# Kernel optimization log

Measured on AMD Instinct MI355X. Metric: run time of the kernel, lower is better.

The kernel has to match this reference:

```python
import jax, jax.numpy as jnp
import numpy as np

N_NODES = 50000
N_EDGES = 640000
F_IN = 16
F_OUT = 16
FCH = 16


def setup_inputs() -> dict:
    key = jax.random.key(0)
    ks = jax.random.split(key, 8)
    x = jax.random.normal(ks[0], (N_NODES, F_IN), dtype=jnp.float32)
    edge_index = jax.random.randint(ks[1], (2, N_EDGES), 0, N_NODES, dtype=jnp.int64)
    edge_vec = jax.random.normal(ks[2], (N_EDGES, 3), dtype=jnp.float32)
    norm = jax.random.uniform(ks[3], (N_EDGES,), dtype=jnp.float32)
    # hypernetwork MLP params: Linear(3, fch) -> ReLU -> Linear(fch, 2*Fin*Fout)
    W1 = jax.random.normal(ks[4], (3, FCH), dtype=jnp.float32) / np.sqrt(3.0)
    b1 = jnp.zeros((FCH,), dtype=jnp.float32)
    W2 = jax.random.normal(ks[5], (FCH, 2 * F_IN * F_OUT), dtype=jnp.float32) / np.sqrt(FCH)
    b2 = jnp.zeros((2 * F_IN * F_OUT,), dtype=jnp.float32)
    return {"x": x, "edge_index": edge_index, "edge_vec": edge_vec, "norm": norm,
            "W1": W1, "b1": b1, "W2": W2, "b2": b2}


def reference(x, edge_index, edge_vec, norm, W1, b1, W2, b2):
    edge_src = edge_index[0]
    edge_dst = edge_index[1]
    # per-edge generated weight matrices: [E, F_OUT, 2*F_IN]
    h = jax.nn.relu(edge_vec @ W1 + b1)
    weights = (h @ W2 + b2).reshape(-1, F_OUT, 2 * F_IN)
    # gather endpoint features and concat: [E, 2*F_IN]
    xe = jnp.concatenate([x[edge_src], x[edge_dst]], axis=1)
    # batched small matmul, tanh activation, norm scaling: [E, F_OUT]
    edge_ftr = jnp.tanh(jnp.einsum('eoi,ei->eo', weights, xe)) * norm[:, None]
    # scatter-add into destination nodes
    return jax.ops.segment_sum(edge_ftr, edge_dst, num_segments=N_NODES)
```

## Files before the change

### kernel.cpp

```cpp
#include <hip/hip_runtime.h>
#include <hip/hip_bf16.h>

#define N_NODES 50000
#define N_EDGES 640000

typedef __attribute__((ext_vector_type(8))) short bf16x8;
typedef __attribute__((ext_vector_type(4))) float f32x4;

static __device__ __forceinline__ short f2bf(float f) {
    __hip_bfloat16 h = __float2bfloat16(f);
    return *reinterpret_cast<const short*>(&h);
}

static __device__ __forceinline__ float sgpr_f(const float* p) {
    return __uint_as_float(__builtin_amdgcn_readfirstlane(__float_as_uint(*p)));
}

__global__ __launch_bounds__(256)
void edge_hyper_kernel(const float* __restrict__ x,
                       const int* __restrict__ ei,
                       const float* __restrict__ ev,
                       const float* __restrict__ nrm,
                       const float* __restrict__ W1,
                       const float* __restrict__ b1,
                       const float* __restrict__ W2,
                       const float* __restrict__ b2,
                       float* __restrict__ out,
                       int ngroups)
{
    __shared__ short w2s[17 * 16 * 34];

    const int tid  = threadIdx.x;
    const int l    = tid & 63;
    const int r    = l & 15;
    const int half = l >> 4;

    for (int idx = tid; idx < 17 * 512; idx += 256) {
        const int c   = idx >> 9;
        const int rem = idx & 511;
        const int o   = rem >> 5;
        const int k   = rem & 31;
        const float v = (c < 16) ? W2[c * 512 + o * 32 + k] : b2[o * 32 + k];
        w2s[(c * 16 + o) * 34 + k] = f2bf(v);
    }

    float w1c0[16], w1c1[16], w1c2[16], b1s[16];
    #pragma unroll
    for (int c = 0; c < 16; ++c) {
        w1c0[c] = sgpr_f(W1 + c);
        w1c1[c] = sgpr_f(W1 + 16 + c);
        w1c2[c] = sgpr_f(W1 + 32 + c);
        b1s[c]  = sgpr_f(b1 + c);
    }

    __syncthreads();

    const short* wbase = &w2s[r * 34 + half * 8];

    const int wv = tid >> 6;
    int g = blockIdx.x * 4 + wv;
    const int nw = gridDim.x * 4;
    if (g >= ngroups) return;

    int    idx_c;
    float4 xa_c, xb_c, nr_c;
    int4   dst_c;
    {
        const int e0 = g * 16;
        idx_c = ei[(half >= 2 ? N_EDGES : 0) + e0 + r];
        nr_c  = *reinterpret_cast<const float4*>(nrm + e0 + half * 4);
        dst_c = *reinterpret_cast<const int4*>(ei + N_EDGES + e0 + half * 4);
        const float4* xr = reinterpret_cast<const float4*>(
            x + (size_t)idx_c * 16 + (half & 1) * 8);
        xa_c = xr[0];
        xb_c = xr[1];
    }

    while (g < ngroups) {
        const int gn   = g + nw;
        const bool hasn = gn < ngroups;
        const int e0   = g * 16;

        const float4* evp = reinterpret_cast<const float4*>(
            ev + (size_t)e0 * 3 + half * 12);
        const float4 ea = evp[0];
        const float4 eb = evp[1];
        const float4 ec = evp[2];

        int    idx_n = 0;
        float4 nr_n = {0.f, 0.f, 0.f, 0.f};
        int4   dst_n = {0, 0, 0, 0};
        if (hasn) {
            const int e0n = gn * 16;
            idx_n = ei[(half >= 2 ? N_EDGES : 0) + e0n + r];
            nr_n  = *reinterpret_cast<const float4*>(nrm + e0n + half * 4);
            dst_n = *reinterpret_cast<const int4*>(ei + N_EDGES + e0n + half * 4);
        }

        bf16x8 afrag;
        afrag[0] = f2bf(xa_c.x); afrag[1] = f2bf(xa_c.y);
        afrag[2] = f2bf(xa_c.z); afrag[3] = f2bf(xa_c.w);
        afrag[4] = f2bf(xb_c.x); afrag[5] = f2bf(xb_c.y);
        afrag[6] = f2bf(xb_c.z); afrag[7] = f2bf(xb_c.w);

        float4 xa_n = {0.f,0.f,0.f,0.f}, xb_n = {0.f,0.f,0.f,0.f};
        if (hasn) {
            const float4* xr = reinterpret_cast<const float4*>(
                x + (size_t)idx_n * 16 + (half & 1) * 8);
            xa_n = xr[0];
            xb_n = xr[1];
        }

        f32x4 s;
        {
            const bf16x8 bfr = *reinterpret_cast<const bf16x8*>(wbase + 16 * 544);
            s = __builtin_amdgcn_mfma_f32_16x16x32_bf16(
                afrag, bfr, (f32x4){0.f, 0.f, 0.f, 0.f}, 0, 0, 0);
        }

        const float ev0[4] = {ea.x, ea.w, eb.z, ec.y};
        const float ev1[4] = {ea.y, eb.x, eb.w, ec.z};
        const float ev2[4] = {ea.z, eb.y, ec.x, ec.w};

        #pragma unroll
        for (int c = 0; c < 16; ++c) {
            const bf16x8 bfr = *reinterpret_cast<const bf16x8*>(wbase + c * 544);
            f32x4 t = __builtin_amdgcn_mfma_f32_16x16x32_bf16(
                afrag, bfr, (f32x4){0.f, 0.f, 0.f, 0.f}, 0, 0, 0);
            #pragma unroll
            for (int q = 0; q < 4; ++q) {
                float hv = fmaf(ev2[q], w1c2[c],
                           fmaf(ev1[q], w1c1[c],
                           fmaf(ev0[q], w1c0[c], b1s[c])));
                hv = fmaxf(hv, 0.0f);
                s[q] = fmaf(hv, t[q], s[q]);
            }
        }

        const float nrv[4] = {nr_c.x, nr_c.y, nr_c.z, nr_c.w};
        const int   dsv[4] = {dst_c.x, dst_c.y, dst_c.z, dst_c.w};
        #pragma unroll
        for (int q = 0; q < 4; ++q) {
            const float sv = s[q];
            const float t  = __expf(-2.0f * fabsf(sv));
            const float th = copysignf((1.0f - t) * __builtin_amdgcn_rcpf(1.0f + t), sv);
            atomicAdd(out + (size_t)dsv[q] * 16 + r, th * nrv[q]);
        }

        idx_c = idx_n;
        nr_c  = nr_n;
        dst_c = dst_n;
        xa_c  = xa_n;
        xb_c  = xb_n;
        g = gn;
    }
}

extern "C" void kernel_launch(void* const* d_in, const int* in_sizes, int n_in,
                              void* d_out, int out_size, void* d_ws, size_t ws_size,
                              hipStream_t stream) {
    const float* x   = (const float*)d_in[0];
    const int*   ei  = (const int*)d_in[1];
    const float* ev  = (const float*)d_in[2];
    const float* nrm = (const float*)d_in[3];
    const float* W1  = (const float*)d_in[4];
    const float* b1  = (const float*)d_in[5];
    const float* W2  = (const float*)d_in[6];
    const float* b2  = (const float*)d_in[7];
    float* out = (float*)d_out;

    hipMemsetAsync(out, 0, (size_t)out_size * sizeof(float), stream);

    const int ngroups = N_EDGES / 16;
    dim3 grid(2048), block(256);
    hipLaunchKernelGGL(edge_hyper_kernel, grid, block, 0, stream,
                       x, ei, ev, nrm, W1, b1, W2, b2, out, ngroups);
}
```

Baseline: 60.30 us.

## Fold hidden activations into MFMA A-operand and accumulate in-chain

Moves the per-edge hidden activation h[c] from a post-MFMA scalar scaling step into the A fragment, so each lane scales its gathered x features by h[c] before the bf16 conversion and the MFMA accumulates directly. Two accumulators alternate to break the MFMA dependency chain. Edge vectors are now loaded per row and prefetched one iteration ahead, and the prefetch is made unconditional by clamping the next index. This removes the per-chunk 4x FMA combine but adds 8 multiplies and bf16 conversions per chunk, and rounds h*x to bf16, which changes precision.

```diff
diff --git a/kernel.cpp b/kernel.cpp
--- a/kernel.cpp
+++ b/kernel.cpp
@@ -63,11 +63,14 @@
     if (g >= ngroups) return;
 
     int    idx_c;
+    float  e0_c, e1_c, e2_c;
     float4 xa_c, xb_c, nr_c;
     int4   dst_c;
     {
         const int e0 = g * 16;
         idx_c = ei[(half >= 2 ? N_EDGES : 0) + e0 + r];
+        const float* evp = ev + (size_t)(e0 + r) * 3;
+        e0_c = evp[0]; e1_c = evp[1]; e2_c = evp[2];
         nr_c  = *reinterpret_cast<const float4*>(nrm + e0 + half * 4);
         dst_c = *reinterpret_cast<const int4*>(ei + N_EDGES + e0 + half * 4);
         const float4* xr = reinterpret_cast<const float4*>(
@@ -77,24 +80,23 @@
     }
 
     while (g < ngroups) {
-        const int gn   = g + nw;
-        const bool hasn = gn < ngroups;
-        const int e0   = g * 16;
+        const int gn    = g + nw;
+        const int gsafe = (gn < ngroups) ? gn : g;
 
-        const float4* evp = reinterpret_cast<const float4*>(
-            ev + (size_t)e0 * 3 + half * 12);
-        const float4 ea = evp[0];
-        const float4 eb = evp[1];
-        const float4 ec = evp[2];
+        const int e0n = gsafe * 16;
+        const int   idx_n = ei[(half >= 2 ? N_EDGES : 0) + e0n + r];
+        const float* evpn = ev + (size_t)(e0n + r) * 3;
+        const float e0_n = evpn[0], e1_n = evpn[1], e2_n = evpn[2];
+        const float4 nr_n = *reinterpret_cast<const float4*>(nrm + e0n + half * 4);
+        const int4   dst_n = *reinterpret_cast<const int4*>(ei + N_EDGES + e0n + half * 4);
 
-        int    idx_n = 0;
-        float4 nr_n = {0.f, 0.f, 0.f, 0.f};
-        int4   dst_n = {0, 0, 0, 0};
-        if (hasn) {
-            const int e0n = gn * 16;
-            idx_n = ei[(half >= 2 ? N_EDGES : 0) + e0n + r];
-            nr_n  = *reinterpret_cast<const float4*>(nrm + e0n + half * 4);
-            dst_n = *reinterpret_cast<const int4*>(ei + N_EDGES + e0n + half * 4);
+        float h[16];
+        #pragma unroll
+        for (int c = 0; c < 16; ++c) {
+            const float hv = fmaf(e2_c, w1c2[c],
+                             fmaf(e1_c, w1c1[c],
+                             fmaf(e0_c, w1c0[c], b1s[c])));
+            h[c] = fmaxf(hv, 0.0f);
         }
 
         bf16x8 afrag;
@@ -103,51 +105,50 @@
         afrag[4] = f2bf(xb_c.x); afrag[5] = f2bf(xb_c.y);
         afrag[6] = f2bf(xb_c.z); afrag[7] = f2bf(xb_c.w);
 
-        float4 xa_n = {0.f,0.f,0.f,0.f}, xb_n = {0.f,0.f,0.f,0.f};
-        if (hasn) {
-            const float4* xr = reinterpret_cast<const float4*>(
-                x + (size_t)idx_n * 16 + (half & 1) * 8);
-            xa_n = xr[0];
-            xb_n = xr[1];
-        }
+        const float4* xrn = reinterpret_cast<const float4*>(
+            x + (size_t)idx_n * 16 + (half & 1) * 8);
+        const float4 xa_n = xrn[0];
+        const float4 xb_n = xrn[1];
 
-        f32x4 s;
+        f32x4 accA, accB;
         {
             const bf16x8 bfr = *reinterpret_cast<const bf16x8*>(wbase + 16 * 544);
-            s = __builtin_amdgcn_mfma_f32_16x16x32_bf16(
+            accA = __builtin_amdgcn_mfma_f32_16x16x32_bf16(
                 afrag, bfr, (f32x4){0.f, 0.f, 0.f, 0.f}, 0, 0, 0);
         }
-
-        const float ev0[4] = {ea.x, ea.w, eb.z, ec.y};
-        const float ev1[4] = {ea.y, eb.x, eb.w, ec.z};
-        const float ev2[4] = {ea.z, eb.y, ec.x, ec.w};
+        accB = (f32x4){0.f, 0.f, 0.f, 0.f};
 
         #pragma unroll
         for (int c = 0; c < 16; ++c) {
             const bf16x8 bfr = *reinterpret_cast<const bf16x8*>(wbase + c * 544);
-            f32x4 t = __builtin_amdgcn_mfma_f32_16x16x32_bf16(
-                afrag, bfr, (f32x4){0.f, 0.f, 0.f, 0.f}, 0, 0, 0);
-            #pragma unroll
-            for (int q = 0; q < 4; ++q) {
-                float hv = fmaf(ev2[q], w1c2[c],
-                           fmaf(ev1[q], w1c1[c],
-                           fmaf(ev0[q], w1c0[c], b1s[c])));
-                hv = fmaxf(hv, 0.0f);
-                s[q] = fmaf(hv, t[q], s[q]);
-            }
+            const float hc = h[c];
+            const float4 y0 = make_float4(hc * xa_c.x, hc * xa_c.y,
+                                          hc * xa_c.z, hc * xa_c.w);
+            const float4 y1 = make_float4(hc * xb_c.x, hc * xb_c.y,
+                                          hc * xb_c.z, hc * xb_c.w);
+            bf16x8 yf;
+            yf[0] = f2bf(y0.x); yf[1] = f2bf(y0.y);
+            yf[2] = f2bf(y0.z); yf[3] = f2bf(y0.w);
+            yf[4] = f2bf(y1.x); yf[5] = f2bf(y1.y);
+            yf[6] = f2bf(y1.z); yf[7] = f2bf(y1.w);
+            if (c & 1)
+                accB = __builtin_amdgcn_mfma_f32_16x16x32_bf16(yf, bfr, accB, 0, 0, 0);
+            else
+                accA = __builtin_amdgcn_mfma_f32_16x16x32_bf16(yf, bfr, accA, 0, 0, 0);
         }
 
         const float nrv[4] = {nr_c.x, nr_c.y, nr_c.z, nr_c.w};
         const int   dsv[4] = {dst_c.x, dst_c.y, dst_c.z, dst_c.w};
         #pragma unroll
         for (int q = 0; q < 4; ++q) {
-            const float sv = s[q];
+            const float sv = accA[q] + accB[q];
             const float t  = __expf(-2.0f * fabsf(sv));
             const float th = copysignf((1.0f - t) * __builtin_amdgcn_rcpf(1.0f + t), sv);
             atomicAdd(out + (size_t)dsv[q] * 16 + r, th * nrv[q]);
         }
 
         idx_c = idx_n;
+        e0_c = e0_n; e1_c = e1_n; e2_c = e2_n;
         nr_c  = nr_n;
         dst_c = dst_n;
         xa_c  = xa_n;
```

Result: faster. 58.49 us (-3.0%).

## Process two edge groups per iteration with deeper index and feature prefetch

Applied to the files above, without the earlier changes.

Each wave now handles two 16-edge groups per loop iteration and interleaves their MFMA chains. Edge indices are prefetched two iterations ahead and gathered node features one iteration ahead. The goal is more memory-level parallelism and independent MFMA work to hide gather latency. The cost is higher register pressure, and out-of-range groups are clamped to valid ones and masked, which adds redundant loads at the tail.

```diff
diff --git a/kernel.cpp b/kernel.cpp
--- a/kernel.cpp
+++ b/kernel.cpp
@@ -58,102 +58,133 @@
     const short* wbase = &w2s[r * 34 + half * 8];
 
     const int wv = tid >> 6;
-    int g = blockIdx.x * 4 + wv;
     const int nw = gridDim.x * 4;
-    if (g >= ngroups) return;
-
-    int    idx_c;
-    float4 xa_c, xb_c, nr_c;
-    int4   dst_c;
+    const int gw = blockIdx.x * 4 + wv;
+    if (gw >= ngroups) return;
+    const int eisel = (half >= 2 ? N_EDGES : 0);
+
+    int gA = gw;
+    int gB = gw + nw;
+
+    #define CLAMPG(G) ((G) < ngroups ? (G) : gw)
+
+    int idxA = ei[eisel + gA * 16 + r];
+    int idxB = ei[eisel + CLAMPG(gB) * 16 + r];
+    float4 xaA, xbA, xaB, xbB;
     {
-        const int e0 = g * 16;
-        idx_c = ei[(half >= 2 ? N_EDGES : 0) + e0 + r];
-        nr_c  = *reinterpret_cast<const float4*>(nrm + e0 + half * 4);
-        dst_c = *reinterpret_cast<const int4*>(ei + N_EDGES + e0 + half * 4);
-        const float4* xr = reinterpret_cast<const float4*>(
-            x + (size_t)idx_c * 16 + (half & 1) * 8);
-        xa_c = xr[0];
-        xb_c = xr[1];
-    }
-
-    while (g < ngroups) {
-        const int gn   = g + nw;
-        const bool hasn = gn < ngroups;
-        const int e0   = g * 16;
-
-        const float4* evp = reinterpret_cast<const float4*>(
-            ev + (size_t)e0 * 3 + half * 12);
-        const float4 ea = evp[0];
-        const float4 eb = evp[1];
-        const float4 ec = evp[2];
-
-        int    idx_n = 0;
-        float4 nr_n = {0.f, 0.f, 0.f, 0.f};
-        int4   dst_n = {0, 0, 0, 0};
-        if (hasn) {
-            const int e0n = gn * 16;
-            idx_n = ei[(half >= 2 ? N_EDGES : 0) + e0n + r];
-            nr_n  = *reinterpret_cast<const float4*>(nrm + e0n + half * 4);
-            dst_n = *reinterpret_cast<const int4*>(ei + N_EDGES + e0n + half * 4);
-        }
-
-        bf16x8 afrag;
-        afrag[0] = f2bf(xa_c.x); afrag[1] = f2bf(xa_c.y);
-        afrag[2] = f2bf(xa_c.z); afrag[3] = f2bf(xa_c.w);
-        afrag[4] = f2bf(xb_c.x); afrag[5] = f2bf(xb_c.y);
-        afrag[6] = f2bf(xb_c.z); afrag[7] = f2bf(xb_c.w);
-
-        float4 xa_n = {0.f,0.f,0.f,0.f}, xb_n = {0.f,0.f,0.f,0.f};
-        if (hasn) {
-            const float4* xr = reinterpret_cast<const float4*>(
-                x + (size_t)idx_n * 16 + (half & 1) * 8);
-            xa_n = xr[0];
-            xb_n = xr[1];
-        }
-
-        f32x4 s;
+        const float4* p = reinterpret_cast<const float4*>(
+            x + (size_t)idxA * 16 + (half & 1) * 8);
+        xaA = p[0]; xbA = p[1];
+        const float4* q = reinterpret_cast<const float4*>(
+            x + (size_t)idxB * 16 + (half & 1) * 8);
+        xaB = q[0]; xbB = q[1];
+    }
+    int idxA1 = ei[eisel + CLAMPG(gA + 2 * nw) * 16 + r];
+    int idxB1 = ei[eisel + CLAMPG(gB + 2 * nw) * 16 + r];
+
+    while (gA < ngroups) {
+        const bool vB = (gB < ngroups);
+        const int gAs = gA;
+        const int gBs = CLAMPG(gB);
+
+        const int idxA2 = ei[eisel + CLAMPG(gA + 4 * nw) * 16 + r];
+        const int idxB2 = ei[eisel + CLAMPG(gB + 4 * nw) * 16 + r];
+
+        const float4* xp1 = reinterpret_cast<const float4*>(
+            x + (size_t)idxA1 * 16 + (half & 1) * 8);
+        const float4 xaA1 = xp1[0];
+        const float4 xbA1 = xp1[1];
+        const float4* xq1 = reinterpret_cast<const float4*>(
+            x + (size_t)idxB1 * 16 + (half & 1) * 8);
+        const float4 xaB1 = xq1[0];
+        const float4 xbB1 = xq1[1];
+
+        const float4* evpA = reinterpret_cast<const float4*>(
+            ev + (size_t)gAs * 48 + half * 12);
+        const float4 eaA = evpA[0], ebA = evpA[1], ecA = evpA[2];
+        const float4* evpB = reinterpret_cast<const float4*>(
+            ev + (size_t)gBs * 48 + half * 12);
+        const float4 eaB = evpB[0], ebB = evpB[1], ecB = evpB[2];
+        const float4 nrA = *reinterpret_cast<const float4*>(nrm + gAs * 16 + half * 4);
+        const float4 nrB = *reinterpret_cast<const float4*>(nrm + gBs * 16 + half * 4);
+        const int4  dstA = *reinterpret_cast<const int4*>(ei + N_EDGES + gAs * 16 + half * 4);
+        const int4  dstB = *reinterpret_cast<const int4*>(ei + N_EDGES + gBs * 16 + half * 4);
+
+        bf16x8 afA, afB;
+        afA[0] = f2bf(xaA.x); afA[1] = f2bf(xaA.y);
+        afA[2] = f2bf(xaA.z); afA[3] = f2bf(xaA.w);
+        afA[4] = f2bf(xbA.x); afA[5] = f2bf(xbA.y);
+        afA[6] = f2bf(xbA.z); afA[7] = f2bf(xbA.w);
+        afB[0] = f2bf(xaB.x); afB[1] = f2bf(xaB.y);
+        afB[2] = f2bf(xaB.z); afB[3] = f2bf(xaB.w);
+        afB[4] = f2bf(xbB.x); afB[5] = f2bf(xbB.y);
+        afB[6] = f2bf(xbB.z); afB[7] = f2bf(xbB.w);
+
+        f32x4 accA, accB;
         {
             const bf16x8 bfr = *reinterpret_cast<const bf16x8*>(wbase + 16 * 544);
-            s = __builtin_amdgcn_mfma_f32_16x16x32_bf16(
-                afrag, bfr, (f32x4){0.f, 0.f, 0.f, 0.f}, 0, 0, 0);
-        }
-
-        const float ev0[4] = {ea.x, ea.w, eb.z, ec.y};
-        const float ev1[4] = {ea.y, eb.x, eb.w, ec.z};
-        const float ev2[4] = {ea.z, eb.y, ec.x, ec.w};
+            accA = __builtin_amdgcn_mfma_f32_16x16x32_bf16(
+                afA, bfr, (f32x4){0.f, 0.f, 0.f, 0.f}, 0, 0, 0);
+            accB = __builtin_amdgcn_mfma_f32_16x16x32_bf16(
+                afB, bfr, (f32x4){0.f, 0.f, 0.f, 0.f}, 0, 0, 0);
+        }
+
+        const float evA0[4] = {eaA.x, eaA.w, ebA.z, ecA.y};
+        const float evA1[4] = {eaA.y, ebA.x, ebA.w, ecA.z};
+        const float evA2[4] = {eaA.z, ebA.y, ecA.x, ecA.w};
+        const float evB0[4] = {eaB.x, eaB.w, ebB.z, ecB.y};
+        const float evB1[4] = {eaB.y, ebB.x, ebB.w, ecB.z};
+        const float evB2[4] = {eaB.z, ebB.y, ecB.x, ecB.w};
 
         #pragma unroll
         for (int c = 0; c < 16; ++c) {
             const bf16x8 bfr = *reinterpret_cast<const bf16x8*>(wbase + c * 544);
-            f32x4 t = __builtin_amdgcn_mfma_f32_16x16x32_bf16(
-                afrag, bfr, (f32x4){0.f, 0.f, 0.f, 0.f}, 0, 0, 0);
+            const f32x4 tA = __builtin_amdgcn_mfma_f32_16x16x32_bf16(
+                afA, bfr, (f32x4){0.f, 0.f, 0.f, 0.f}, 0, 0, 0);
+            const f32x4 tB = __builtin_amdgcn_mfma_f32_16x16x32_bf16(
+                afB, bfr, (f32x4){0.f, 0.f, 0.f, 0.f}, 0, 0, 0);
             #pragma unroll
             for (int q = 0; q < 4; ++q) {
-                float hv = fmaf(ev2[q], w1c2[c],
-                           fmaf(ev1[q], w1c1[c],
-                           fmaf(ev0[q], w1c0[c], b1s[c])));
-                hv = fmaxf(hv, 0.0f);
-                s[q] = fmaf(hv, t[q], s[q]);
+                float hA = fmaf(evA2[q], w1c2[c],
+                           fmaf(evA1[q], w1c1[c],
+                           fmaf(evA0[q], w1c0[c], b1s[c])));
+                hA = fmaxf(hA, 0.0f);
+                accA[q] = fmaf(hA, tA[q], accA[q]);
+                float hB = fmaf(evB2[q], w1c2[c],
+                           fmaf(evB1[q], w1c1[c],
+                           fmaf(evB0[q], w1c0[c], b1s[c])));
+                hB = fmaxf(hB, 0.0f);
+                accB[q] = fmaf(hB, tB[q], accB[q]);
             }
         }
 
-        const float nrv[4] = {nr_c.x, nr_c.y, nr_c.z, nr_c.w};
-        const int   dsv[4] = {dst_c.x, dst_c.y, dst_c.z, dst_c.w};
         #pragma unroll
         for (int q = 0; q < 4; ++q) {
-            const float sv = s[q];
+            const float sv = accA[q];
             const float t  = __expf(-2.0f * fabsf(sv));
             const float th = copysignf((1.0f - t) * __builtin_amdgcn_rcpf(1.0f + t), sv);
-            atomicAdd(out + (size_t)dsv[q] * 16 + r, th * nrv[q]);
-        }
-
-        idx_c = idx_n;
-        nr_c  = nr_n;
-        dst_c = dst_n;
-        xa_c  = xa_n;
-        xb_c  = xb_n;
-        g = gn;
-    }
+            const float* nr4 = reinterpret_cast<const float*>(&nrA);
+            const int*   ds4 = reinterpret_cast<const int*>(&dstA);
+            atomicAdd(out + (size_t)ds4[q] * 16 + r, th * nr4[q]);
+        }
+        if (vB) {
+            #pragma unroll
+            for (int q = 0; q < 4; ++q) {
+                const float sv = accB[q];
+                const float t  = __expf(-2.0f * fabsf(sv));
+                const float th = copysignf((1.0f - t) * __builtin_amdgcn_rcpf(1.0f + t), sv);
+                const float* nr4 = reinterpret_cast<const float*>(&nrB);
+                const int*   ds4 = reinterpret_cast<const int*>(&dstB);
+                atomicAdd(out + (size_t)ds4[q] * 16 + r, th * nr4[q]);
+            }
+        }
+
+        xaA = xaA1; xbA = xbA1; xaB = xaB1; xbB = xbB1;
+        idxA1 = idxA2; idxB1 = idxB2;
+        gA += 2 * nw;
+        gB += 2 * nw;
+    }
+    #undef CLAMPG
 }
 
 extern "C" void kernel_launch(void* const* d_in, const int* in_sizes, int n_in,
```

New measurement: 91.19 us. +51.2%, slower.
